# Optimization experiments

Hardware: AMD Instinct MI355X
Metric: run time of the kernel (lower is better)

## Reference

```python
import jax, jax.numpy as jnp
import numpy as np

TOP_K = 0.7  # fraction of highest-loss samples kept


def setup_inputs() -> dict:
    key = jax.random.key(0)
    k1, k2 = jax.random.split(key)
    N, C = 262144, 128
    inp = jax.random.normal(k1, (N, C), dtype=jnp.float32)
    tgt = jax.random.randint(k2, (N,), 0, C, dtype=jnp.int64)
    return {"input": inp, "target": tgt}


def reference(input, target):
    # log-softmax over classes, one stable pass
    logp = jax.nn.log_softmax(input, axis=-1)  # [N, C]
    # per-row NLL: -logp[i, target[i]]
    per_row = -jnp.take_along_axis(logp, target[:, None], axis=-1)[:, 0]  # [N]
    k = int(TOP_K * per_row.shape[0])
    top_vals, _ = jax.lax.top_k(per_row, k)  # k largest losses
    return jnp.mean(top_vals)
```

## Files before the change

kernel.cpp:

```cpp
#include <hip/hip_runtime.h>


#define NCLASS 128
#define NREP 8
#define TPB 256
#define REF_GRID 256

struct Scalars {
  unsigned sel1;
  unsigned cnt_above;
  int krem;
};

__device__ __forceinline__ unsigned suffix_incl_u(unsigned x, int lane) {
#pragma unroll
  for (int off = 1; off < 64; off <<= 1) {
    unsigned v = __shfl_down(x, off, 64);
    if (lane + off < 64) x += v;
  }
  return x;
}

__device__ __forceinline__ double xor_reduce_d(double x) {
#pragma unroll
  for (int off = 32; off > 0; off >>= 1) x += __shfl_xor(x, off, 64);
  return x;
}

__device__ __forceinline__ void scan_desc(const unsigned* __restrict__ hist,
                                          int nbins, int nrep, unsigned Ktar,
                                          int* bin_out, unsigned* above_out) {
  const int lane = threadIdx.x;
  const int bpt = nbins >> 6;
  unsigned csum = 0;
  for (int rr = 0; rr < nrep; ++rr) {
    const unsigned* hp = hist + (size_t)rr * nbins + lane * bpt;
    for (int i = 0; i < bpt; ++i) csum += hp[i];
  }
  unsigned suf = suffix_incl_u(csum, lane);
  unsigned long long mask = __ballot(suf >= Ktar);
  int c = 63 - __builtin_clzll(mask);
  unsigned aboveC = __shfl(suf - csum, c, 64);

  unsigned h = 0;
  if (lane < bpt)
    for (int rr = 0; rr < nrep; ++rr)
      h += hist[(size_t)rr * nbins + c * bpt + lane];
  unsigned suf2 = suffix_incl_u(h, lane);
  unsigned long long mask2 = __ballot((lane < bpt) && (aboveC + suf2 >= Ktar));
  int u = 63 - __builtin_clzll(mask2);
  unsigned above = aboveC + __shfl(suf2 - h, u, 64);
  *bin_out = c * bpt + u;
  *above_out = above;
}

__global__ __launch_bounds__(TPB) void loss_hist_kernel(
    const float* __restrict__ x, const int* __restrict__ tgt,
    float* __restrict__ losses, unsigned* __restrict__ hist1, int N) {
  __shared__ unsigned lh[4096];
  for (int i = threadIdx.x; i < 4096; i += TPB) lh[i] = 0;
  __syncthreads();

  const int lane = threadIdx.x & 63;
  const int j = lane & 3;
  const int r = lane >> 2;
  const int wave = blockIdx.x * (TPB / 64) + (threadIdx.x >> 6);
  const int row = wave * 16 + r;

  const float4* rp = (const float4*)(x + (size_t)row * NCLASS);
  float4 v0 = rp[j];
  float4 v1 = rp[j + 4];
  float4 v2 = rp[j + 8];
  float4 v3 = rp[j + 12];
  float4 v4 = rp[j + 16];
  float4 v5 = rp[j + 20];
  float4 v6 = rp[j + 24];
  float4 v7 = rp[j + 28];
  float xt = 0.0f;
  if (j == 0) {
    int t = tgt[row];
    xt = x[(size_t)row * NCLASS + t];
  }

  float m = fmaxf(fmaxf(fmaxf(v0.x, v0.y), fmaxf(v0.z, v0.w)),
                  fmaxf(fmaxf(v1.x, v1.y), fmaxf(v1.z, v1.w)));
  m = fmaxf(m, fmaxf(fmaxf(fmaxf(v2.x, v2.y), fmaxf(v2.z, v2.w)),
                     fmaxf(fmaxf(v3.x, v3.y), fmaxf(v3.z, v3.w))));
  m = fmaxf(m, fmaxf(fmaxf(fmaxf(v4.x, v4.y), fmaxf(v4.z, v4.w)),
                     fmaxf(fmaxf(v5.x, v5.y), fmaxf(v5.z, v5.w))));
  m = fmaxf(m, fmaxf(fmaxf(fmaxf(v6.x, v6.y), fmaxf(v6.z, v6.w)),
                     fmaxf(fmaxf(v7.x, v7.y), fmaxf(v7.z, v7.w))));
  m = fmaxf(m, __shfl_xor(m, 1, 64));
  m = fmaxf(m, __shfl_xor(m, 2, 64));

  float s = __expf(v0.x - m) + __expf(v0.y - m) + __expf(v0.z - m) + __expf(v0.w - m)
          + __expf(v1.x - m) + __expf(v1.y - m) + __expf(v1.z - m) + __expf(v1.w - m)
          + __expf(v2.x - m) + __expf(v2.y - m) + __expf(v2.z - m) + __expf(v2.w - m)
          + __expf(v3.x - m) + __expf(v3.y - m) + __expf(v3.z - m) + __expf(v3.w - m)
          + __expf(v4.x - m) + __expf(v4.y - m) + __expf(v4.z - m) + __expf(v4.w - m)
          + __expf(v5.x - m) + __expf(v5.y - m) + __expf(v5.z - m) + __expf(v5.w - m)
          + __expf(v6.x - m) + __expf(v6.y - m) + __expf(v6.z - m) + __expf(v6.w - m)
          + __expf(v7.x - m) + __expf(v7.y - m) + __expf(v7.z - m) + __expf(v7.w - m);
  s += __shfl_xor(s, 1, 64);
  s += __shfl_xor(s, 2, 64);

  if (j == 0) {
    float loss = fmaxf(__logf(s) + m - xt, 0.0f);
    losses[row] = loss;
    atomicAdd(&lh[__float_as_uint(loss) >> 20], 1u);
  }
  __syncthreads();
  unsigned* h = hist1 + (size_t)(blockIdx.x & (NREP - 1)) * 4096;
  for (int i = threadIdx.x; i < 4096; i += TPB) {
    unsigned v = lh[i];
    if (v) atomicAdd(&h[i], v);
  }
}

__global__ __launch_bounds__(TPB) void refine_kernel(
    const float* __restrict__ losses, const unsigned* __restrict__ hist1,
    unsigned* __restrict__ hist2, float* __restrict__ hsum2,
    unsigned* __restrict__ fine, Scalars* __restrict__ sc,
    double* __restrict__ partials, int N, int K) {
  __shared__ unsigned lc[1024];
  __shared__ float lsum[1024];
  __shared__ double dsm[TPB / 64];
  __shared__ unsigned sel1_sh;
  for (int i = threadIdx.x; i < 1024; i += TPB) { lc[i] = 0; lsum[i] = 0.0f; }

  if (threadIdx.x < 64) {
    int bin; unsigned above;
    scan_desc(hist1, 4096, NREP, (unsigned)K, &bin, &above);
    if (threadIdx.x == 0) {
      sel1_sh = (unsigned)bin;
      if (blockIdx.x == 0) {
        sc->sel1 = (unsigned)bin;
        sc->cnt_above = above;
        sc->krem = K - (int)above;
      }
    }
  }
  __syncthreads();

  const int lane = threadIdx.x & 63;
  const unsigned sel1 = sel1_sh;
  const float4* L4 = (const float4*)losses;
  const int n4 = N >> 2;
  double accS1 = 0.0;
  for (int idx = blockIdx.x * TPB + threadIdx.x; idx < n4;
       idx += REF_GRID * TPB) {
    float4 v = L4[idx];
#pragma unroll
    for (int comp = 0; comp < 4; ++comp) {
      float f = (comp == 0) ? v.x : (comp == 1) ? v.y : (comp == 2) ? v.z : v.w;
      unsigned b = __float_as_uint(f);
      unsigned hi = b >> 20;
      if (hi > sel1) {
        accS1 += (double)f;
      } else if (hi == sel1) {
        atomicAdd(&lc[(b >> 10) & 1023u], 1u);
        atomicAdd(&lsum[(b >> 10) & 1023u], f);
        atomicAdd(&fine[b & 0xFFFFFu], 1u);
      }
    }
  }
  accS1 = xor_reduce_d(accS1);
  if (lane == 0) dsm[threadIdx.x >> 6] = accS1;
  __syncthreads();
  if (threadIdx.x == 0)
    partials[blockIdx.x] = dsm[0] + dsm[1] + dsm[2] + dsm[3];

  unsigned* h = hist2 + (size_t)(blockIdx.x & (NREP - 1)) * 1024;
  for (int i = threadIdx.x; i < 1024; i += TPB) {
    unsigned c = lc[i];
    if (c) { atomicAdd(&h[i], c); atomicAdd(&hsum2[i], lsum[i]); }
  }
}

__global__ __launch_bounds__(TPB) void final_kernel(
    const unsigned* __restrict__ hist2, const float* __restrict__ hsum2,
    const unsigned* __restrict__ fine, const Scalars* __restrict__ sc,
    const double* __restrict__ partials, float* __restrict__ out, int K) {
  __shared__ double dsm[TPB / 64];
  __shared__ double S1sh;
  const int lane = threadIdx.x & 63;

  double s1 = partials[threadIdx.x];
  s1 = xor_reduce_d(s1);
  if (lane == 0) dsm[threadIdx.x >> 6] = s1;
  __syncthreads();
  if (threadIdx.x == 0) S1sh = dsm[0] + dsm[1] + dsm[2] + dsm[3];
  __syncthreads();

  if (threadIdx.x < 64) {
    const unsigned sel1 = sc->sel1;
    const unsigned krem = (unsigned)sc->krem;
    int sel2; unsigned above2;
    scan_desc(hist2, 1024, NREP, krem, &sel2, &above2);
    const unsigned krem2 = krem - above2;

    double s2 = 0.0;
    for (int b = sel2 + 1 + lane; b < 1024; b += 64) s2 += (double)hsum2[b];
    s2 = xor_reduce_d(s2);

    const unsigned* freg = fine + ((size_t)sel2 << 10);
    int bin3; unsigned above3;
    scan_desc(freg, 1024, 1, krem2, &bin3, &above3);

    const unsigned pfx = (sel1 << 20) | ((unsigned)sel2 << 10);
    double s3 = 0.0;
    for (int t = bin3 + 1 + lane; t < 1024; t += 64) {
      unsigned c = freg[t];
      if (c) s3 += (double)c * (double)__uint_as_float(pfx | (unsigned)t);
    }
    s3 = xor_reduce_d(s3);

    if (lane == 0) {
      unsigned thr_bits = pfx | (unsigned)bin3;
      unsigned cnt_gt = sc->cnt_above + above2 + above3;
      double thrv = (double)__uint_as_float(thr_bits);
      double mean = (S1sh + s2 + s3 +
                     (double)(K - (int)cnt_gt) * thrv) / (double)K;
      *out = (float)mean;
    }
  }
}

extern "C" void kernel_launch(void* const* d_in, const int* in_sizes, int n_in,
                              void* d_out, int out_size, void* d_ws, size_t ws_size,
                              hipStream_t stream) {
  const float* x = (const float*)d_in[0];
  const int* tgt = (const int*)d_in[1];
  float* out = (float*)d_out;
  int N = in_sizes[1];
  int K = (int)(0.7 * (double)N);

  char* ws = (char*)d_ws;
  const size_t OFF_H1 = (size_t)N * 4;
  const size_t OFF_H2 = OFF_H1 + (size_t)NREP * 4096 * 4;
  const size_t OFF_HS = OFF_H2 + (size_t)NREP * 1024 * 4;
  const size_t OFF_SC = OFF_HS + 1024 * 4;
  const size_t OFF_FN = OFF_SC + 128;
  const size_t OFF_PT = OFF_FN + (size_t)(1u << 20) * 4;

  float* losses = (float*)ws;
  unsigned* hist1 = (unsigned*)(ws + OFF_H1);
  unsigned* hist2 = (unsigned*)(ws + OFF_H2);
  float* hsum2 = (float*)(ws + OFF_HS);
  Scalars* sc = (Scalars*)(ws + OFF_SC);
  unsigned* fine = (unsigned*)(ws + OFF_FN);
  double* partials = (double*)(ws + OFF_PT);

  hipMemsetAsync(ws + OFF_H1, 0, OFF_PT - OFF_H1, stream);

  loss_hist_kernel<<<N / 64, TPB, 0, stream>>>(x, tgt, losses, hist1, N);
  refine_kernel<<<REF_GRID, TPB, 0, stream>>>(losses, hist1, hist2, hsum2,
                                              fine, sc, partials, N, K);
  final_kernel<<<1, TPB, 0, stream>>>(hist2, hsum2, fine, sc, partials, out, K);
}
```

Measured before the change: 211.4 us.

## Use nontemporal loads, pick target logit from registers, fold zeroing into kernel

```diff
diff --git a/kernel.cpp b/kernel.cpp
--- a/kernel.cpp
+++ b/kernel.cpp
@@ -5,6 +5,8 @@
 #define NREP 8
 #define TPB 256
 #define REF_GRID 256
+
+typedef float v4f __attribute__((ext_vector_type(4)));
 
 struct Scalars {
   unsigned sel1;
@@ -56,10 +58,10 @@
 
 __global__ __launch_bounds__(TPB) void loss_hist_kernel(
     const float* __restrict__ x, const int* __restrict__ tgt,
-    float* __restrict__ losses, unsigned* __restrict__ hist1, int N) {
+    float* __restrict__ losses, unsigned* __restrict__ hist1,
+    unsigned* __restrict__ zbase, int zwords, int N) {
   __shared__ unsigned lh[4096];
   for (int i = threadIdx.x; i < 4096; i += TPB) lh[i] = 0;
-  __syncthreads();
 
   const int lane = threadIdx.x & 63;
   const int j = lane & 3;
@@ -67,20 +69,40 @@
   const int wave = blockIdx.x * (TPB / 64) + (threadIdx.x >> 6);
   const int row = wave * 16 + r;
 
-  const float4* rp = (const float4*)(x + (size_t)row * NCLASS);
-  float4 v0 = rp[j];
-  float4 v1 = rp[j + 4];
-  float4 v2 = rp[j + 8];
-  float4 v3 = rp[j + 12];
-  float4 v4 = rp[j + 16];
-  float4 v5 = rp[j + 20];
-  float4 v6 = rp[j + 24];
-  float4 v7 = rp[j + 28];
+  const v4f* rp = (const v4f*)(x + (size_t)row * NCLASS);
+  v4f v0 = __builtin_nontemporal_load(rp + j);
+  v4f v1 = __builtin_nontemporal_load(rp + j + 4);
+  v4f v2 = __builtin_nontemporal_load(rp + j + 8);
+  v4f v3 = __builtin_nontemporal_load(rp + j + 12);
+  v4f v4 = __builtin_nontemporal_load(rp + j + 16);
+  v4f v5 = __builtin_nontemporal_load(rp + j + 20);
+  v4f v6 = __builtin_nontemporal_load(rp + j + 24);
+  v4f v7 = __builtin_nontemporal_load(rp + j + 28);
+  int t = (j == 0) ? tgt[row] : 0;
+
+  for (int i = blockIdx.x * TPB + threadIdx.x; i < zwords;
+       i += gridDim.x * TPB)
+    zbase[i] = 0;
+
+  __syncthreads();
+
+  t = __shfl(t, lane & ~3, 64);
   float xt = 0.0f;
-  if (j == 0) {
-    int t = tgt[row];
-    xt = x[(size_t)row * NCLASS + t];
-  }
+  if (((t >> 2) & 3) == j) {
+    const int k = t >> 4;
+    v4f a = (k & 1) ? v1 : v0;
+    v4f b = (k & 1) ? v3 : v2;
+    v4f c = (k & 1) ? v5 : v4;
+    v4f d = (k & 1) ? v7 : v6;
+    v4f e = (k & 2) ? b : a;
+    v4f f = (k & 2) ? d : c;
+    v4f g = (k & 4) ? f : e;
+    float lo = (t & 1) ? g.y : g.x;
+    float hi = (t & 1) ? g.w : g.z;
+    xt = (t & 2) ? hi : lo;
+  }
+  xt += __shfl_xor(xt, 1, 64);
+  xt += __shfl_xor(xt, 2, 64);
 
   float m = fmaxf(fmaxf(fmaxf(v0.x, v0.y), fmaxf(v0.z, v0.w)),
                   fmaxf(fmaxf(v1.x, v1.y), fmaxf(v1.z, v1.w)));
@@ -251,9 +273,12 @@
   unsigned* fine = (unsigned*)(ws + OFF_FN);
   double* partials = (double*)(ws + OFF_PT);
 
-  hipMemsetAsync(ws + OFF_H1, 0, OFF_PT - OFF_H1, stream);
-
-  loss_hist_kernel<<<N / 64, TPB, 0, stream>>>(x, tgt, losses, hist1, N);
+  (void)hipMemsetAsync(ws + OFF_H1, 0, OFF_H2 - OFF_H1, stream);
+
+  const int zwords = (int)((OFF_PT - OFF_H2) / 4);
+  loss_hist_kernel<<<N / 64, TPB, 0, stream>>>(x, tgt, losses, hist1,
+                                               (unsigned*)(ws + OFF_H2),
+                                               zwords, N);
   refine_kernel<<<REF_GRID, TPB, 0, stream>>>(losses, hist1, hist2, hsum2,
                                               fine, sc, partials, N, K);
   final_kernel<<<1, TPB, 0, stream>>>(hist2, hsum2, fine, sc, partials, out, K);
```

After: 207.6 us. No clear change (-1.8%).
